# Performance work log

Measured on AMD Instinct MI355X. Metric: run time of the kernel, lower is better.

The kernel has to match this reference:

```python
import jax, jax.numpy as jnp
import numpy as np

E = 400000   # n_entity
R = 500      # n_relation
D = 128      # embed_dim
B = 2048     # batch of queries
K = 128      # sample_limit (refer neighbors per query)
GAMMA = 24.0
EPS = 2.0


def _xavier(key, fan_out, fan_in):
    lim = np.sqrt(6.0 / (fan_in + fan_out)).astype(np.float32)
    return jax.random.uniform(key, (fan_out, fan_in), minval=-lim, maxval=lim, dtype=jnp.float32)


def setup_inputs() -> dict:
    key = jax.random.key(0)
    ks = jax.random.split(key, 9)
    erange = (GAMMA + EPS) / D
    # tables with the appended zero padding row (as in forward's torch.cat)
    ent = jax.random.uniform(ks[0], (E + R + 1, D), minval=-erange, maxval=erange, dtype=jnp.float32)
    entity_embedding = jnp.concatenate([ent, jnp.zeros((1, D), jnp.float32)], axis=0)
    rel = jax.random.uniform(ks[1], (R + 1, D), minval=-erange, maxval=erange, dtype=jnp.float32)
    relation_embedding = jnp.concatenate([rel, jnp.zeros((1, D), jnp.float32)], axis=0)
    off = jax.random.uniform(ks[2], (R + 1, D), minval=0.0, maxval=erange, dtype=jnp.float32)
    offset_embedding = jnp.concatenate([off, jnp.zeros((1, D), jnp.float32)], axis=0)
    # ProjectionAggregating attention MLP params
    W1 = _xavier(ks[3], D, 2 * D)
    b1 = jnp.zeros((D,), jnp.float32)
    W2 = _xavier(ks[4], D, D)
    b2 = jnp.zeros((D,), jnp.float32)
    anchors = jax.random.randint(ks[5], (B,), 0, E)
    rel_0 = jax.random.randint(ks[6], (B,), 0, R)
    p1_target = jax.random.randint(ks[7], (B, K), 0, E)
    p1_rel = jax.random.randint(ks[8], (B, K), 0, R)
    return {
        'entity_embedding': entity_embedding,
        'relation_embedding': relation_embedding,
        'offset_embedding': offset_embedding,
        'W1': W1, 'b1': b1, 'W2': W2, 'b2': b2,
        'anchors': anchors, 'rel_0': rel_0,
        'p1_target': p1_target, 'p1_rel': p1_rel,
    }


def reference(entity_embedding, relation_embedding, offset_embedding,
              W1, b1, W2, b2, anchors, rel_0, p1_target, p1_rel):
    # ---- '1p' query path of IDN_Q2B_24.forward ----
    h_a = entity_embedding[anchors]            # [B, D]
    r_q = relation_embedding[rel_0]            # [B, D]
    query_emb = h_a + r_q                      # [B, D]
    offset_emb = offset_embedding[rel_0]       # [B, D]  (activation = Identity)
    h_t = entity_embedding[p1_target]          # [B, K, D]  refer_embs
    r_t = relation_embedding[p1_rel]           # [B, K, D]  refer_r
    # ProjectionAggregating (aggr='bias'): bias = refer - (start + refer_r)
    bias = h_t - (h_a[:, None, :] + r_t)       # [B, K, D]
    x = jnp.concatenate([r_t, jnp.broadcast_to(r_q[:, None, :], r_t.shape)], axis=-1)  # [B,K,2D]
    a1 = jax.nn.relu(jnp.einsum('bkf,df->bkd', x, W1) + b1)   # [B, K, D]
    attn = jnp.einsum('bkd,ed->bke', a1, W2) + b2             # [B, K, D]
    final_refer = jnp.sum(attn * bias, axis=-2)               # [B, D]
    final_query = query_emb + final_refer
    return final_query, offset_emb
```

## Files before the change

kernel.cpp:

```cpp
#include <hip/hip_runtime.h>

typedef __attribute__((ext_vector_type(8))) short short8;
typedef __attribute__((ext_vector_type(4))) float f32x4;

#define NRELROWS 502
#define NB 2048
#define DD 128
#define OUT_HALF (NB * DD)

__device__ __forceinline__ short f2bf(float x) {
    union { float f; unsigned u; } c; c.f = x;
    return (short)((c.u + 0x7FFFu + ((c.u >> 16) & 1u)) >> 16);
}

__global__ __launch_bounds__(256) void precompute_kernel(
    const float* __restrict__ rel, const float* __restrict__ W1,
    const float* __restrict__ b1, const float* __restrict__ W2,
    float* __restrict__ U, float* __restrict__ V,
    unsigned short* __restrict__ W2f)
{
    const int bid = blockIdx.x;
    const int tid = threadIdx.x;
    if (bid < 126) {
        __shared__ float srel[4][DD];
        const int r0 = bid << 2;
        for (int i = tid; i < 512; i += 256) {
            const int r = i >> 7, c = i & 127;
            const int rr = r0 + r;
            srel[r][c] = (rr < NRELROWS) ? rel[rr * DD + c] : 0.f;
        }
        __syncthreads();
        const int half = tid >> 7;
        const int d = tid & 127;
        const float* wrow = W1 + d * 256 + half * 128;
        float a0 = 0.f, a1 = 0.f, a2 = 0.f, a3 = 0.f;
#pragma unroll 8
        for (int f = 0; f < 128; f += 4) {
            const float4 wv = *(const float4*)(wrow + f);
            a0 += srel[0][f]*wv.x + srel[0][f+1]*wv.y + srel[0][f+2]*wv.z + srel[0][f+3]*wv.w;
            a1 += srel[1][f]*wv.x + srel[1][f+1]*wv.y + srel[1][f+2]*wv.z + srel[1][f+3]*wv.w;
            a2 += srel[2][f]*wv.x + srel[2][f+1]*wv.y + srel[2][f+2]*wv.z + srel[2][f+3]*wv.w;
            a3 += srel[3][f]*wv.x + srel[3][f+1]*wv.y + srel[3][f+2]*wv.z + srel[3][f+3]*wv.w;
        }
        float res[4] = {a0, a1, a2, a3};
        const float bb = half ? b1[d] : 0.f;
#pragma unroll
        for (int r = 0; r < 4; ++r) {
            if (r0 + r < NRELROWS) {
                if (half) V[(r0 + r) * DD + d] = res[r] + bb;
                else      U[(r0 + r) * DD + d] = res[r];
            }
        }
    } else {
        const int tile = bid - 126;
        const int kt = tile >> 3, nt = tile & 7;
#pragma unroll
        for (int e = 0; e < 2; ++e) {
            const int within = tid * 2 + e;
            const int l = within >> 3, i = within & 7;
            const int n = nt * 16 + (l & 15);
            const int f = kt * 32 + (l >> 4) * 8 + i;
            W2f[tile * 512 + within] = (unsigned short)f2bf(W2[n * 128 + f]);
        }
    }
}

__global__ __launch_bounds__(256) void main_kernel(
    const float* __restrict__ ent, const float* __restrict__ rel,
    const float* __restrict__ off, const float* __restrict__ b2,
    const int* __restrict__ anchors, const int* __restrict__ rel0,
    const int* __restrict__ p1t, const int* __restrict__ p1r,
    const float* __restrict__ U, const float* __restrict__ V,
    const unsigned short* __restrict__ W2f, float* __restrict__ out)
{
    __shared__ float ht[4][32][DD];
    const int b = blockIdx.x;
    const int tid = threadIdx.x;
    const int w = tid >> 6;
    const int l = tid & 63;
    const int lg = l >> 4;
    const int l15 = l & 15;
    const int half = l >> 5;

    const int aidx = anchors[b];
    const int r0 = rel0[b];
    const int* p1t_b = p1t + (b << 7);
    const int* p1r_b = p1r + (b << 7);

    int rowi[16];
#pragma unroll
    for (int j = 0; j < 16; ++j)
        rowi[j] = p1t_b[(w << 5) + (j << 1) + half];
#pragma unroll
    for (int j = 0; j < 16; ++j) {
        const float* g = ent + (size_t)rowi[j] * DD + ((l & 31) << 2);
        float* lp = &ht[w][j << 1][0];
        __builtin_amdgcn_global_load_lds(
            (const __attribute__((address_space(1))) unsigned int*)g,
            (__attribute__((address_space(3))) unsigned int*)lp, 16, 0, 0);
    }

    int relA[2];
    relA[0] = p1r_b[(w << 5) + l15];
    relA[1] = p1r_b[(w << 5) + 16 + l15];

    f32x4 acc[2][8];
#pragma unroll
    for (int t = 0; t < 2; ++t)
#pragma unroll
        for (int n = 0; n < 8; ++n) acc[t][n] = (f32x4)0.f;

    const float* Vrow = V + r0 * DD;

#pragma unroll
    for (int kt = 0; kt < 4; ++kt) {
        const int f0 = kt * 32 + lg * 8;
        const float4 vv0 = *(const float4*)(Vrow + f0);
        const float4 vv1 = *(const float4*)(Vrow + f0 + 4);
        short8 af[2];
#pragma unroll
        for (int t = 0; t < 2; ++t) {
            const float* Urow = U + relA[t] * DD + f0;
            const float4 u0 = *(const float4*)(Urow);
            const float4 u1 = *(const float4*)(Urow + 4);
            af[t][0] = f2bf(fmaxf(u0.x + vv0.x, 0.f));
            af[t][1] = f2bf(fmaxf(u0.y + vv0.y, 0.f));
            af[t][2] = f2bf(fmaxf(u0.z + vv0.z, 0.f));
            af[t][3] = f2bf(fmaxf(u0.w + vv0.w, 0.f));
            af[t][4] = f2bf(fmaxf(u1.x + vv1.x, 0.f));
            af[t][5] = f2bf(fmaxf(u1.y + vv1.y, 0.f));
            af[t][6] = f2bf(fmaxf(u1.z + vv1.z, 0.f));
            af[t][7] = f2bf(fmaxf(u1.w + vv1.w, 0.f));
        }
        const unsigned short* Wk = W2f + (kt << 3) * 512 + (l << 3);
#pragma unroll
        for (int nt = 0; nt < 8; ++nt) {
            const short8 bf = *(const short8*)(Wk + (nt << 9));
            acc[0][nt] = __builtin_amdgcn_mfma_f32_16x16x32_bf16(af[0], bf, acc[0][nt], 0, 0, 0);
            acc[1][nt] = __builtin_amdgcn_mfma_f32_16x16x32_bf16(af[1], bf, acc[1][nt], 0, 0, 0);
        }
    }

    int rr[2][4];
#pragma unroll
    for (int t = 0; t < 2; ++t) {
        const int4 r4 = *(const int4*)(p1r_b + (w << 5) + (t << 4) + (lg << 2));
        rr[t][0] = r4.x; rr[t][1] = r4.y; rr[t][2] = r4.z; rr[t][3] = r4.w;
    }
    const float* arow = ent + (size_t)aidx * DD;

    asm volatile("s_waitcnt vmcnt(0)" ::: "memory");
    __builtin_amdgcn_sched_barrier(0);

    float ps[8];
#pragma unroll
    for (int nt = 0; nt < 8; ++nt) ps[nt] = 0.f;
#pragma unroll
    for (int nt = 0; nt < 8; ++nt) {
        const int d = (nt << 4) + l15;
        const float had = arow[d];
        const float b2d = b2[d];
#pragma unroll
        for (int t = 0; t < 2; ++t) {
#pragma unroll
            for (int r2 = 0; r2 < 4; ++r2) {
                const float at = acc[t][nt][r2] + b2d;
                const float htv = ht[w][(t << 4) + (lg << 2) + r2][d];
                const float rtv = rel[rr[t][r2] * DD + d];
                ps[nt] += at * (htv - had - rtv);
            }
        }
        ps[nt] += __shfl_xor(ps[nt], 16);
        ps[nt] += __shfl_xor(ps[nt], 32);
    }

    __syncthreads();
    float* red = &ht[0][0][0];
    if (lg == 0) {
#pragma unroll
        for (int nt = 0; nt < 8; ++nt)
            red[w * DD + (nt << 4) + l15] = ps[nt];
    }
    __syncthreads();
    if (tid < DD) {
        const int d = tid;
        const float s = red[d] + red[DD + d] + red[2 * DD + d] + red[3 * DD + d];
        out[(b << 7) + d] = arow[d] + rel[r0 * DD + d] + s;
        out[OUT_HALF + (b << 7) + d] = off[r0 * DD + d];
    }
}

extern "C" void kernel_launch(void* const* d_in, const int* in_sizes, int n_in,
                              void* d_out, int out_size, void* d_ws, size_t ws_size,
                              hipStream_t stream) {
    const float* ent  = (const float*)d_in[0];
    const float* rel  = (const float*)d_in[1];
    const float* off  = (const float*)d_in[2];
    const float* W1   = (const float*)d_in[3];
    const float* b1   = (const float*)d_in[4];
    const float* W2   = (const float*)d_in[5];
    const float* b2   = (const float*)d_in[6];
    const int* anchors = (const int*)d_in[7];
    const int* rel0    = (const int*)d_in[8];
    const int* p1t     = (const int*)d_in[9];
    const int* p1r     = (const int*)d_in[10];
    float* out = (float*)d_out;

    float* U = (float*)d_ws;
    float* V = U + NRELROWS * DD;
    unsigned short* W2f = (unsigned short*)(V + NRELROWS * DD);

    precompute_kernel<<<126 + 32, 256, 0, stream>>>(rel, W1, b1, W2, U, V, W2f);
    main_kernel<<<NB, 256, 0, stream>>>(ent, rel, off, b2, anchors, rel0,
                                        p1t, p1r, U, V, W2f, out);
}
```

Before: 56.68 us.

## Stage W2 tiles in LDS and gather entity rows directly into registers

The main kernel no longer stages gathered entity rows in a 64KB LDS buffer. It copies the bf16 W2 fragment tiles into 32KB of LDS once per block and loads the entity and relation rows straight into registers, processing the two 16-row subtiles one after the other. Output-only loads are hoisted to the start, and launch bounds now request 3 blocks per SM. The goal is lower LDS use and higher occupancy, at the cost of uncoalesced 4-byte gathers (16 lanes each reading strided floats) and more register pressure.

```diff
diff --git a/kernel.cpp b/kernel.cpp
--- a/kernel.cpp
+++ b/kernel.cpp
@@ -65,7 +65,7 @@
     }
 }
 
-__global__ __launch_bounds__(256) void main_kernel(
+__global__ __launch_bounds__(256, 3) void main_kernel(
     const float* __restrict__ ent, const float* __restrict__ rel,
     const float* __restrict__ off, const float* __restrict__ b2,
     const int* __restrict__ anchors, const int* __restrict__ rel0,
@@ -73,120 +73,134 @@
     const float* __restrict__ U, const float* __restrict__ V,
     const unsigned short* __restrict__ W2f, float* __restrict__ out)
 {
-    __shared__ float ht[4][32][DD];
+    __shared__ unsigned short w2l[32 * 512];
+    __shared__ float red[4][DD];
     const int b = blockIdx.x;
     const int tid = threadIdx.x;
     const int w = tid >> 6;
     const int l = tid & 63;
     const int lg = l >> 4;
     const int l15 = l & 15;
-    const int half = l >> 5;
 
     const int aidx = anchors[b];
     const int r0 = rel0[b];
     const int* p1t_b = p1t + (b << 7);
     const int* p1r_b = p1r + (b << 7);
 
-    int rowi[16];
-#pragma unroll
-    for (int j = 0; j < 16; ++j)
-        rowi[j] = p1t_b[(w << 5) + (j << 1) + half];
-#pragma unroll
-    for (int j = 0; j < 16; ++j) {
-        const float* g = ent + (size_t)rowi[j] * DD + ((l & 31) << 2);
-        float* lp = &ht[w][j << 1][0];
+    float o_a = 0.f, o_r = 0.f, o_o = 0.f;
+    if (tid < DD) {
+        o_a = ent[(size_t)aidx * DD + tid];
+        o_r = rel[r0 * DD + tid];
+        o_o = off[r0 * DD + tid];
+    }
+    float hav[8], b2v[8];
+    const float* ar = ent + (size_t)aidx * DD + l15;
+#pragma unroll
+    for (int nt = 0; nt < 8; ++nt) {
+        hav[nt] = ar[nt << 4];
+        b2v[nt] = b2[(nt << 4) + l15];
+    }
+    int relA[2];
+    int4 tg4[2], rr4[2];
+#pragma unroll
+    for (int t = 0; t < 2; ++t) {
+        const int base = (w << 5) + (t << 4);
+        relA[t] = p1r_b[base + l15];
+        tg4[t] = *(const int4*)(p1t_b + base + (lg << 2));
+        rr4[t] = *(const int4*)(p1r_b + base + (lg << 2));
+    }
+#pragma unroll
+    for (int i = 0; i < 8; ++i) {
+        const int chunk = (w << 3) + i;
+        const unsigned short* g = W2f + chunk * 512 + (l << 3);
+        unsigned short* lp = w2l + chunk * 512;
         __builtin_amdgcn_global_load_lds(
             (const __attribute__((address_space(1))) unsigned int*)g,
             (__attribute__((address_space(3))) unsigned int*)lp, 16, 0, 0);
     }
-
-    int relA[2];
-    relA[0] = p1r_b[(w << 5) + l15];
-    relA[1] = p1r_b[(w << 5) + 16 + l15];
-
-    f32x4 acc[2][8];
-#pragma unroll
-    for (int t = 0; t < 2; ++t)
-#pragma unroll
-        for (int n = 0; n < 8; ++n) acc[t][n] = (f32x4)0.f;
+    asm volatile("s_waitcnt vmcnt(0) lgkmcnt(0)" ::: "memory");
+    __builtin_amdgcn_s_barrier();
+
+    float p[8];
+#pragma unroll
+    for (int nt = 0; nt < 8; ++nt) p[nt] = 0.f;
 
     const float* Vrow = V + r0 * DD;
 
 #pragma unroll
-    for (int kt = 0; kt < 4; ++kt) {
-        const int f0 = kt * 32 + lg * 8;
-        const float4 vv0 = *(const float4*)(Vrow + f0);
-        const float4 vv1 = *(const float4*)(Vrow + f0 + 4);
-        short8 af[2];
-#pragma unroll
-        for (int t = 0; t < 2; ++t) {
-            const float* Urow = U + relA[t] * DD + f0;
-            const float4 u0 = *(const float4*)(Urow);
-            const float4 u1 = *(const float4*)(Urow + 4);
-            af[t][0] = f2bf(fmaxf(u0.x + vv0.x, 0.f));
-            af[t][1] = f2bf(fmaxf(u0.y + vv0.y, 0.f));
-            af[t][2] = f2bf(fmaxf(u0.z + vv0.z, 0.f));
-            af[t][3] = f2bf(fmaxf(u0.w + vv0.w, 0.f));
-            af[t][4] = f2bf(fmaxf(u1.x + vv1.x, 0.f));
-            af[t][5] = f2bf(fmaxf(u1.y + vv1.y, 0.f));
-            af[t][6] = f2bf(fmaxf(u1.z + vv1.z, 0.f));
-            af[t][7] = f2bf(fmaxf(u1.w + vv1.w, 0.f));
-        }
-        const unsigned short* Wk = W2f + (kt << 3) * 512 + (l << 3);
+    for (int t = 0; t < 2; ++t) {
+        const float* Urow = U + relA[t] * DD;
+        short8 af[4];
+#pragma unroll
+        for (int kt = 0; kt < 4; ++kt) {
+            const int f0 = kt * 32 + lg * 8;
+            const float4 u0 = *(const float4*)(Urow + f0);
+            const float4 u1 = *(const float4*)(Urow + f0 + 4);
+            const float4 v0 = *(const float4*)(Vrow + f0);
+            const float4 v1 = *(const float4*)(Vrow + f0 + 4);
+            af[kt][0] = f2bf(fmaxf(u0.x + v0.x, 0.f));
+            af[kt][1] = f2bf(fmaxf(u0.y + v0.y, 0.f));
+            af[kt][2] = f2bf(fmaxf(u0.z + v0.z, 0.f));
+            af[kt][3] = f2bf(fmaxf(u0.w + v0.w, 0.f));
+            af[kt][4] = f2bf(fmaxf(u1.x + v1.x, 0.f));
+            af[kt][5] = f2bf(fmaxf(u1.y + v1.y, 0.f));
+            af[kt][6] = f2bf(fmaxf(u1.z + v1.z, 0.f));
+            af[kt][7] = f2bf(fmaxf(u1.w + v1.w, 0.f));
+        }
+        __builtin_amdgcn_sched_barrier(0);
+
+        const int tg[4] = {tg4[t].x, tg4[t].y, tg4[t].z, tg4[t].w};
+        const int rr[4] = {rr4[t].x, rr4[t].y, rr4[t].z, rr4[t].w};
+        float htv[4][8], rvv[4][8];
+#pragma unroll
+        for (int r2 = 0; r2 < 4; ++r2) {
+            const float* gp = ent + (size_t)tg[r2] * DD + l15;
+            const float* rp = rel + rr[r2] * DD + l15;
+#pragma unroll
+            for (int nt = 0; nt < 8; ++nt) {
+                htv[r2][nt] = gp[nt << 4];
+                rvv[r2][nt] = rp[nt << 4];
+            }
+        }
+        __builtin_amdgcn_sched_barrier(0);
+
+        f32x4 acc[8];
+#pragma unroll
+        for (int nt = 0; nt < 8; ++nt) acc[nt] = (f32x4)0.f;
+#pragma unroll
+        for (int kt = 0; kt < 4; ++kt) {
+#pragma unroll
+            for (int nt = 0; nt < 8; ++nt) {
+                const short8 bf = *(const short8*)(w2l + ((kt << 3) + nt) * 512 + (l << 3));
+                acc[nt] = __builtin_amdgcn_mfma_f32_16x16x32_bf16(af[kt], bf, acc[nt], 0, 0, 0);
+            }
+        }
+
 #pragma unroll
         for (int nt = 0; nt < 8; ++nt) {
-            const short8 bf = *(const short8*)(Wk + (nt << 9));
-            acc[0][nt] = __builtin_amdgcn_mfma_f32_16x16x32_bf16(af[0], bf, acc[0][nt], 0, 0, 0);
-            acc[1][nt] = __builtin_amdgcn_mfma_f32_16x16x32_bf16(af[1], bf, acc[1][nt], 0, 0, 0);
-        }
-    }
-
-    int rr[2][4];
-#pragma unroll
-    for (int t = 0; t < 2; ++t) {
-        const int4 r4 = *(const int4*)(p1r_b + (w << 5) + (t << 4) + (lg << 2));
-        rr[t][0] = r4.x; rr[t][1] = r4.y; rr[t][2] = r4.z; rr[t][3] = r4.w;
-    }
-    const float* arow = ent + (size_t)aidx * DD;
-
-    asm volatile("s_waitcnt vmcnt(0)" ::: "memory");
-    __builtin_amdgcn_sched_barrier(0);
-
-    float ps[8];
-#pragma unroll
-    for (int nt = 0; nt < 8; ++nt) ps[nt] = 0.f;
+#pragma unroll
+            for (int r2 = 0; r2 < 4; ++r2) {
+                const float at = acc[nt][r2] + b2v[nt];
+                p[nt] += at * (htv[r2][nt] - hav[nt] - rvv[r2][nt]);
+            }
+        }
+    }
+
 #pragma unroll
     for (int nt = 0; nt < 8; ++nt) {
-        const int d = (nt << 4) + l15;
-        const float had = arow[d];
-        const float b2d = b2[d];
-#pragma unroll
-        for (int t = 0; t < 2; ++t) {
-#pragma unroll
-            for (int r2 = 0; r2 < 4; ++r2) {
-                const float at = acc[t][nt][r2] + b2d;
-                const float htv = ht[w][(t << 4) + (lg << 2) + r2][d];
-                const float rtv = rel[rr[t][r2] * DD + d];
-                ps[nt] += at * (htv - had - rtv);
-            }
-        }
-        ps[nt] += __shfl_xor(ps[nt], 16);
-        ps[nt] += __shfl_xor(ps[nt], 32);
-    }
-
-    __syncthreads();
-    float* red = &ht[0][0][0];
+        p[nt] += __shfl_xor(p[nt], 16);
+        p[nt] += __shfl_xor(p[nt], 32);
+    }
     if (lg == 0) {
 #pragma unroll
         for (int nt = 0; nt < 8; ++nt)
-            red[w * DD + (nt << 4) + l15] = ps[nt];
+            red[w][(nt << 4) + l15] = p[nt];
     }
     __syncthreads();
     if (tid < DD) {
-        const int d = tid;
-        const float s = red[d] + red[DD + d] + red[2 * DD + d] + red[3 * DD + d];
-        out[(b << 7) + d] = arow[d] + rel[r0 * DD + d] + s;
-        out[OUT_HALF + (b << 7) + d] = off[r0 * DD + d];
+        const float s = red[0][tid] + red[1][tid] + red[2][tid] + red[3][tid];
+        out[(b << 7) + tid] = o_a + o_r + s;
+        out[OUT_HALF + (b << 7) + tid] = o_o;
     }
 }
 
```

Result: slower. 88.40 us (+55.9%).
